# Performance work log

Measured on AMD Instinct MI355X. Metric: run time of the kernel, lower is better.

Reference implementation:

```python
import jax, jax.numpy as jnp
import numpy as np

B, C_IN, C_OUT, H, W = 4, 256, 256, 56, 56
NH, K, P = 2, 5, 2
HD = C_OUT // NH          # 128
SE_H = C_OUT // 16        # 16
SE_H2 = max(SE_H // 16, 1)  # 1
EPS = 1e-5


def setup_inputs() -> dict:
    key = jax.random.key(0)
    ks = jax.random.split(key, 16)
    n = lambda k, sh, s=1.0: jax.random.normal(k, sh, jnp.float32) * s

    def bn_params(k, c):
        k1, k2 = jax.random.split(k)
        return (1.0 + 0.1 * n(k1, (c,)), 0.1 * n(k2, (c,)),
                jnp.zeros((c,), jnp.float32), jnp.ones((c,), jnp.float32))

    agg_g1, agg_b1, agg_m1, agg_v1 = bn_params(ks[6], C_OUT)
    agg_g2, agg_b2, agg_m2, agg_v2 = bn_params(ks[7], C_OUT)
    se_g_in, se_b_in, se_m_in, se_v_in = bn_params(ks[8], SE_H)
    se_g_out, se_b_out, se_m_out, se_v_out = bn_params(ks[9], C_OUT)
    return {
        "x": n(ks[0], (B, C_IN, H, W)),
        "Wq": n(ks[1], (C_OUT, C_IN), C_IN ** -0.5),
        "Wk": n(ks[2], (C_OUT, C_IN), C_IN ** -0.5),
        "Wv": n(ks[3], (C_OUT, C_IN), C_IN ** -0.5),
        "rel_h": n(ks[4], (HD, 1, 1, K, 1)),
        "rel_w": n(ks[5], (HD, 1, 1, 1, K)),
        "agg_g1": agg_g1, "agg_b1": agg_b1, "agg_m1": agg_m1, "agg_v1": agg_v1,
        "agg_W": n(ks[10], (C_OUT, C_OUT), C_OUT ** -0.5),
        "agg_g2": agg_g2, "agg_b2": agg_b2, "agg_m2": agg_m2, "agg_v2": agg_v2,
        "se_Win": n(ks[11], (SE_H, C_OUT), C_OUT ** -0.5),
        "se_g_in": se_g_in, "se_b_in": se_b_in, "se_m_in": se_m_in, "se_v_in": se_v_in,
        "se_fc1": n(ks[12], (SE_H2, SE_H), SE_H ** -0.5),
        "se_fc2": n(ks[13], (SE_H, SE_H2)),
        "se_Wout": n(ks[14], (C_OUT, SE_H), SE_H ** -0.5),
        "se_g_out": se_g_out, "se_b_out": se_b_out, "se_m_out": se_m_out, "se_v_out": se_v_out,
    }


def _conv1x1(Wm, t):
    return jnp.einsum('oc,bchw->bohw', Wm, t)


def _bn(t, g, b, m, v):
    # eval-mode BatchNorm2d with running stats
    return (t - m[:, None, None]) * (g * jax.lax.rsqrt(v + EPS))[:, None, None] + b[:, None, None]


def _windows(t):
    # (B, O, H+2P, W+2P) -> (B, O, H, W, K, K), matching torch unfold(2,K,1).unfold(3,K,1)
    w = jnp.stack([t[:, :, i:i + H, j:j + W] for i in range(K) for j in range(K)], axis=-1)
    return w.reshape(t.shape[0], t.shape[1], H, W, K, K)


def reference(x, Wq, Wk, Wv, rel_h, rel_w,
              agg_g1, agg_b1, agg_m1, agg_v1, agg_W, agg_g2, agg_b2, agg_m2, agg_v2,
              se_Win, se_g_in, se_b_in, se_m_in, se_v_in, se_fc1, se_fc2, se_Wout,
              se_g_out, se_b_out, se_m_out, se_v_out):
    xp = jnp.pad(x, ((0, 0), (0, 0), (P, P), (P, P)))
    q = _conv1x1(Wq, x).reshape(B, NH, HD, H, W)          # (B,NH,HD,H,W)
    k_win = _windows(_conv1x1(Wk, xp))                    # (B,O,H,W,K,K)
    v_win = _windows(_conv1x1(Wv, xp))
    # relative position bias: first head gets rel_h (height taps), second gets rel_w
    k_win = jnp.concatenate([k_win[:, :HD] + rel_h[None], k_win[:, HD:] + rel_w[None]], axis=1)
    k_r = k_win.reshape(B, NH, HD, H, W, K * K)
    v_r = v_win.reshape(B, NH, HD, H, W, K * K)
    scores = jnp.einsum('bnchw,bnchwk->bnhwk', q, k_r) / jnp.sqrt(jnp.float32(HD))
    attn = jax.nn.softmax(scores, axis=-1)
    out = jnp.einsum('bnhwk,bnchwk->bnchw', attn, v_r).reshape(B, C_OUT, H, W)
    # agg: BN -> ReLU -> 1x1 conv -> BN
    y = jax.nn.relu(_bn(out, agg_g1, agg_b1, agg_m1, agg_v1))
    y = _bn(_conv1x1(agg_W, y), agg_g2, agg_b2, agg_m2, agg_v2)
    # squeeze-excitation (intended math; original view(b,c) is a channel-count bug)
    s = jax.nn.relu(_bn(_conv1x1(se_Win, y), se_g_in, se_b_in, se_m_in, se_v_in))  # (B,SE_H,H,W)
    p = s.mean(axis=(2, 3))                                                        # (B,SE_H)
    g = jax.nn.sigmoid(jax.nn.relu(p @ se_fc1.T) @ se_fc2.T)                       # (B,SE_H)
    s = s * g[:, :, None, None]
    return _bn(_conv1x1(se_Wout, s), se_g_out, se_b_out, se_m_out, se_v_out)
```

## Files before the change

kernel.cpp:

```cpp
#include <hip/hip_runtime.h>
#include <hip/hip_bf16.h>

#define HW 3136
#define HH 56
#define WW 56
#define BB 4
#define CC 256
#define HD 128

#define TH 4
#define TW 8
#define WR 8
#define WC 12
#define WPX 96
#define KSTR 132
#define SSTR 33

#define ASTR 72

typedef __attribute__((ext_vector_type(8))) short bf16x8;
typedef __attribute__((ext_vector_type(4))) float f32x4;

__device__ __forceinline__ unsigned short f2bf(float f) {
    unsigned int u; __builtin_memcpy(&u, &f, 4);
    unsigned int r = u + 0x7FFFu + ((u >> 16) & 1u);
    return (unsigned short)(r >> 16);
}
__device__ __forceinline__ float bflo(unsigned int u) {
    unsigned int x = u << 16; float f; __builtin_memcpy(&f, &x, 4); return f;
}
__device__ __forceinline__ float bfhi(unsigned int u) {
    unsigned int x = u & 0xFFFF0000u; float f; __builtin_memcpy(&f, &x, 4); return f;
}

__global__ __launch_bounds__(256) void xt_cvt(const float* __restrict__ x,
                                              unsigned short* __restrict__ xt)
{
    int b = blockIdx.z;
    int c0 = blockIdx.y * 64;
    int p0 = blockIdx.x * 64;
    __shared__ float tile[64][65];
    int t = threadIdx.x;
    int p4 = t & 15, cl = t >> 4;
    const float* xb = x + ((size_t)b * CC + c0) * HW + p0;
#pragma unroll
    for (int i = 0; i < 4; i++) {
        int c = cl + 16 * i;
        float4 f = *(const float4*)(xb + (size_t)c * HW + p4 * 4);
        tile[c][p4 * 4 + 0] = f.x; tile[c][p4 * 4 + 1] = f.y;
        tile[c][p4 * 4 + 2] = f.z; tile[c][p4 * 4 + 3] = f.w;
    }
    __syncthreads();
    int c2 = t & 31, pl = t >> 5;
    unsigned short* xo = xt + ((size_t)b * HW + p0) * CC + c0;
#pragma unroll
    for (int i = 0; i < 8; i++) {
        int p = pl + 8 * i;
        float a = tile[2 * c2][p], bb = tile[2 * c2 + 1][p];
        unsigned int pk = (unsigned int)f2bf(a) | ((unsigned int)f2bf(bb) << 16);
        *(unsigned int*)(xo + (size_t)p * CC + 2 * c2) = pk;
    }
}

__global__ __launch_bounds__(256) void wcvt(const float* __restrict__ Wq,
                                            const float* __restrict__ Wk,
                                            const float* __restrict__ Wv,
                                            const float* __restrict__ Wa,
                                            unsigned short* __restrict__ wb)
{
    const float* srcs[4] = {Wq, Wk, Wv, Wa};
    const float* s = srcs[blockIdx.y];
    int idx = blockIdx.x * 256 + threadIdx.x;
    float4 f = *(const float4*)(s + (size_t)idx * 4);
    uint2 pk;
    pk.x = (unsigned int)f2bf(f.x) | ((unsigned int)f2bf(f.y) << 16);
    pk.y = (unsigned int)f2bf(f.z) | ((unsigned int)f2bf(f.w) << 16);
    *(uint2*)(wb + (size_t)blockIdx.y * 65536 + (size_t)idx * 4) = pk;
}

__global__ __launch_bounds__(256) void qkv_mfma(
    const unsigned short* __restrict__ xt, const unsigned short* __restrict__ wqkv,
    unsigned short* __restrict__ q_ws, unsigned short* __restrict__ k_ws,
    unsigned short* __restrict__ v_ws)
{
    int wsel = blockIdx.z;
    unsigned short* outp = (wsel == 0) ? q_ws : ((wsel == 1) ? k_ws : v_ws);
    int gp0 = blockIdx.x * 128, o0 = blockIdx.y * 128;

    __shared__ unsigned short As[128 * ASTR];
    __shared__ unsigned short Bs[128 * ASTR];
    const unsigned short* xb = xt + (size_t)gp0 * CC;
    const unsigned short* wbp = wqkv + (size_t)wsel * 65536 + (size_t)o0 * CC;

    int t = threadIdx.x;
    int wave = t >> 6, lane = t & 63;
    int mo = (wave & 1) * 64, no = (wave >> 1) * 64;
    int lm = lane & 15, lq = lane >> 4;
    int sr = t >> 3, sc = t & 7;

    f32x4 acc[4][4];
#pragma unroll
    for (int i = 0; i < 4; i++)
#pragma unroll
        for (int j = 0; j < 4; j++) acc[i][j] = (f32x4){0.f, 0.f, 0.f, 0.f};

    for (int k0 = 0; k0 < 256; k0 += 64) {
#pragma unroll
        for (int i = 0; i < 4; i++) {
            int r = sr + 32 * i;
            *(uint4*)&As[r * ASTR + sc * 8] = *(const uint4*)(xb + (size_t)r * CC + k0 + sc * 8);
            *(uint4*)&Bs[r * ASTR + sc * 8] = *(const uint4*)(wbp + (size_t)r * CC + k0 + sc * 8);
        }
        __syncthreads();
#pragma unroll
        for (int ks = 0; ks < 64; ks += 32) {
            bf16x8 af[4], bfr[4];
#pragma unroll
            for (int i = 0; i < 4; i++)
                af[i] = *(bf16x8*)&As[(mo + 16 * i + lm) * ASTR + ks + lq * 8];
#pragma unroll
            for (int j = 0; j < 4; j++)
                bfr[j] = *(bf16x8*)&Bs[(no + 16 * j + lm) * ASTR + ks + lq * 8];
#pragma unroll
            for (int i = 0; i < 4; i++)
#pragma unroll
                for (int j = 0; j < 4; j++)
                    acc[i][j] = __builtin_amdgcn_mfma_f32_16x16x32_bf16(
                        af[i], bfr[j], acc[i][j], 0, 0, 0);
        }
        __syncthreads();
    }
    unsigned short* ob = outp + (size_t)gp0 * CC + o0;
    bool ev = (lm & 1) == 0;
    int elm = lm & ~1;
#pragma unroll
    for (int i = 0; i < 4; i++)
#pragma unroll
        for (int j = 0; j < 4; j++)
#pragma unroll
            for (int r = 0; r < 4; r++) {
                float v = acc[i][j][r];
                float p = __shfl_xor(v, 1, 64);
                unsigned int pk = ev
                    ? ((unsigned int)f2bf(v) | ((unsigned int)f2bf(p) << 16))
                    : ((unsigned int)f2bf(p) | ((unsigned int)f2bf(v) << 16));
                if (ev == (r < 2)) {
                    int m = mo + 16 * i + lq * 4 + r;
                    int n = no + 16 * j + elm;
                    *(unsigned int*)(ob + (size_t)m * CC + n) = pk;
                }
            }
}

__global__ __launch_bounds__(256) void agg_mfma(
    const unsigned short* __restrict__ ao, const unsigned short* __restrict__ wagg,
    const float* __restrict__ g1, const float* __restrict__ b1,
    const float* __restrict__ m1, const float* __restrict__ v1,
    const float* __restrict__ g2, const float* __restrict__ b2,
    const float* __restrict__ m2, const float* __restrict__ v2,
    float* __restrict__ y2)
{
    int gp0 = blockIdx.x * 128, o0 = blockIdx.y * 128;

    __shared__ unsigned short As[128 * ASTR];
    __shared__ unsigned short Bs[128 * ASTR];
    __shared__ float s1[256], o1[256], s2[256], o2[256];

    int t = threadIdx.x;
    {
        float sc1 = g1[t] * rsqrtf(v1[t] + 1e-5f);
        s1[t] = sc1; o1[t] = b1[t] - m1[t] * sc1;
        float sc2 = g2[t] * rsqrtf(v2[t] + 1e-5f);
        s2[t] = sc2; o2[t] = b2[t] - m2[t] * sc2;
    }

    const unsigned short* aob = ao + (size_t)gp0 * CC;
    const unsigned short* wbp = wagg + (size_t)o0 * CC;

    int wave = t >> 6, lane = t & 63;
    int mo = (wave & 1) * 64, no = (wave >> 1) * 64;
    int lm = lane & 15, lq = lane >> 4;
    int sr = t >> 3, sc = t & 7;

    f32x4 acc[4][4];
#pragma unroll
    for (int i = 0; i < 4; i++)
#pragma unroll
        for (int j = 0; j < 4; j++) acc[i][j] = (f32x4){0.f, 0.f, 0.f, 0.f};

    __syncthreads();

    for (int k0 = 0; k0 < 256; k0 += 64) {
#pragma unroll
        for (int i = 0; i < 4; i++) {
            int r = sr + 32 * i;
            int cb = k0 + sc * 8;
            uint4 u = *(const uint4*)(aob + (size_t)r * CC + cb);
            float e[8] = {bflo(u.x), bfhi(u.x), bflo(u.y), bfhi(u.y),
                          bflo(u.z), bfhi(u.z), bflo(u.w), bfhi(u.w)};
            unsigned short pk[8];
#pragma unroll
            for (int uu = 0; uu < 8; uu++) {
                float vv = fmaxf(e[uu] * s1[cb + uu] + o1[cb + uu], 0.f);
                pk[uu] = f2bf(vv);
            }
            *(uint4*)&As[r * ASTR + sc * 8] = *(uint4*)pk;
            *(uint4*)&Bs[r * ASTR + sc * 8] = *(const uint4*)(wbp + (size_t)r * CC + k0 + sc * 8);
        }
        __syncthreads();
#pragma unroll
        for (int ks = 0; ks < 64; ks += 32) {
            bf16x8 af[4], bfr[4];
#pragma unroll
            for (int i = 0; i < 4; i++)
                af[i] = *(bf16x8*)&As[(mo + 16 * i + lm) * ASTR + ks + lq * 8];
#pragma unroll
            for (int j = 0; j < 4; j++)
                bfr[j] = *(bf16x8*)&Bs[(no + 16 * j + lm) * ASTR + ks + lq * 8];
#pragma unroll
            for (int i = 0; i < 4; i++)
#pragma unroll
                for (int j = 0; j < 4; j++)
                    acc[i][j] = __builtin_amdgcn_mfma_f32_16x16x32_bf16(
                        af[i], bfr[j], acc[i][j], 0, 0, 0);
        }
        __syncthreads();
    }
    float* yb = y2 + (size_t)gp0 * CC + o0;
#pragma unroll
    for (int i = 0; i < 4; i++)
#pragma unroll
        for (int j = 0; j < 4; j++)
#pragma unroll
            for (int r = 0; r < 4; r++) {
                int m = mo + 16 * i + lq * 4 + r;
                int n = no + 16 * j + lm;
                yb[(size_t)m * CC + n] = acc[i][j][r] * s2[o0 + n] + o2[o0 + n];
            }
}

__global__ __launch_bounds__(256) void attn_kernel(
    const unsigned short* __restrict__ q_ws, const unsigned short* __restrict__ k_ws,
    const unsigned short* __restrict__ v_ws,
    const float* __restrict__ rel_h, const float* __restrict__ rel_w,
    unsigned short* __restrict__ ao_ws)
{
    __shared__ float kwin[WPX * KSTR];
    __shared__ float sbuf[32 * SSTR];
    __shared__ float relT[5 * KSTR];

    int t = threadIdx.x;
    int tile = blockIdx.x;
    int n = blockIdx.y;
    int b = blockIdx.z;
    int tr = tile / 7, tc = tile - tr * 7;
    int h0 = tr * TH, w0 = tc * TW;
    const float* rel = (n == 0) ? rel_h : rel_w;
    const size_t base = (size_t)b * HW * CC + n * HD;

    {
        int c8 = t & 15, pw0 = t >> 4;
#pragma unroll
        for (int it = 0; it < 6; it++) {
            int pw = pw0 + it * 16;
            int wr = pw / 12, wc = pw - wr * 12;
            int gh = h0 + wr - 2, gw = w0 + wc - 2;
            float f[8] = {0.f, 0.f, 0.f, 0.f, 0.f, 0.f, 0.f, 0.f};
            if (gh >= 0 && gh < HH && gw >= 0 && gw < WW) {
                uint4 u = *(const uint4*)(k_ws + base + (size_t)(gh * WW + gw) * CC + c8 * 8);
                f[0] = bflo(u.x); f[1] = bfhi(u.x); f[2] = bflo(u.y); f[3] = bfhi(u.y);
                f[4] = bflo(u.z); f[5] = bfhi(u.z); f[6] = bflo(u.w); f[7] = bfhi(u.w);
            }
            *(float4*)&kwin[pw * KSTR + c8 * 8]     = make_float4(f[0], f[1], f[2], f[3]);
            *(float4*)&kwin[pw * KSTR + c8 * 8 + 4] = make_float4(f[4], f[5], f[6], f[7]);
        }
        if (t < 128) {
#pragma unroll
            for (int tt = 0; tt < 5; tt++)
                relT[tt * KSTR + t] = rel[t * 5 + tt];
        }
    }
    __syncthreads();

    int px = t >> 3, c4g = t & 7;
    int pr = px >> 3, pc = px & 7;
    int ghp = h0 + pr, gwp = w0 + pc;
    const size_t pbase = base + (size_t)(ghp * WW + gwp) * CC;

    float4 q4[4];
#pragma unroll
    for (int i = 0; i < 4; i++) {
        uint2 uq = *(const uint2*)(q_ws + pbase + (c4g + 8 * i) * 4);
        q4[i] = make_float4(bflo(uq.x), bfhi(uq.x), bflo(uq.y), bfhi(uq.y));
    }

    float acc[30];
#pragma unroll
    for (int tt = 0; tt < 30; tt++) acc[tt] = 0.f;
#pragma unroll
    for (int i = 0; i < 4; i++) {
        float4 q = q4[i];
        int co = (c4g + 8 * i) * 4;
#pragma unroll
        for (int tt = 0; tt < 25; tt++) {
            int di = tt / 5, dj = tt - 5 * (tt / 5);
            int wpx = (pr + di) * WC + pc + dj;
            float4 k4 = *(const float4*)&kwin[wpx * KSTR + co];
            acc[tt] += q.x * k4.x + q.y * k4.y + q.z * k4.z + q.w * k4.w;
        }
#pragma unroll
        for (int tt = 0; tt < 5; tt++) {
            float4 r4 = *(const float4*)&relT[tt * KSTR + co];
            acc[25 + tt] += q.x * r4.x + q.y * r4.y + q.z * r4.z + q.w * r4.w;
        }
    }
#pragma unroll
    for (int tt = 0; tt < 30; tt++) {
#pragma unroll
        for (int m = 1; m < 8; m <<= 1)
            acc[tt] += __shfl_xor(acc[tt], m, 64);
    }
#pragma unroll
    for (int tt = 0; tt < 30; tt++)
        if ((tt & 7) == c4g) sbuf[px * SSTR + tt] = acc[tt];
    __syncthreads();

    {
        int c8 = t & 15, pw0 = t >> 4;
#pragma unroll
        for (int it = 0; it < 6; it++) {
            int pw = pw0 + it * 16;
            int wr = pw / 12, wc = pw - wr * 12;
            int gh = h0 + wr - 2, gw = w0 + wc - 2;
            float f[8] = {0.f, 0.f, 0.f, 0.f, 0.f, 0.f, 0.f, 0.f};
            if (gh >= 0 && gh < HH && gw >= 0 && gw < WW) {
                uint4 u = *(const uint4*)(v_ws + base + (size_t)(gh * WW + gw) * CC + c8 * 8);
                f[0] = bflo(u.x); f[1] = bfhi(u.x); f[2] = bflo(u.y); f[3] = bfhi(u.y);
                f[4] = bflo(u.z); f[5] = bfhi(u.z); f[6] = bflo(u.w); f[7] = bfhi(u.w);
            }
            *(float4*)&kwin[pw * KSTR + c8 * 8]     = make_float4(f[0], f[1], f[2], f[3]);
            *(float4*)&kwin[pw * KSTR + c8 * 8 + 4] = make_float4(f[4], f[5], f[6], f[7]);
        }
    }
    if (t < 32) {
        float s[25], b5[5];
#pragma unroll
        for (int tt = 0; tt < 25; tt++) s[tt] = sbuf[t * SSTR + tt];
#pragma unroll
        for (int tt = 0; tt < 5; tt++) b5[tt] = sbuf[t * SSTR + 25 + tt];
        const float inv = 0.08838834764831845f;
        float mx = -1e30f;
#pragma unroll
        for (int tt = 0; tt < 25; tt++) {
            int di = tt / 5, dj = tt - 5 * (tt / 5);
            s[tt] = (s[tt] + ((n == 0) ? b5[di] : b5[dj])) * inv;
            mx = fmaxf(mx, s[tt]);
        }
        float sum = 0.f;
#pragma unroll
        for (int tt = 0; tt < 25; tt++) { s[tt] = __expf(s[tt] - mx); sum += s[tt]; }
        float rs = 1.f / sum;
#pragma unroll
        for (int tt = 0; tt < 25; tt++) sbuf[t * SSTR + tt] = s[tt] * rs;
    }
    __syncthreads();

    float w25[25];
#pragma unroll
    for (int tt = 0; tt < 25; tt++) w25[tt] = sbuf[px * SSTR + tt];
    float4 oacc[4];
#pragma unroll
    for (int i = 0; i < 4; i++) oacc[i] = make_float4(0.f, 0.f, 0.f, 0.f);
#pragma unroll
    for (int tt = 0; tt < 25; tt++) {
        int di = tt / 5, dj = tt - 5 * (tt / 5);
        int wpx = (pr + di) * WC + pc + dj;
        float a = w25[tt];
#pragma unroll
        for (int i = 0; i < 4; i++) {
            float4 v4 = *(const float4*)&kwin[wpx * KSTR + (c4g + 8 * i) * 4];
            oacc[i].x += a * v4.x; oacc[i].y += a * v4.y;
            oacc[i].z += a * v4.z; oacc[i].w += a * v4.w;
        }
    }
#pragma unroll
    for (int i = 0; i < 4; i++) {
        uint2 pk;
        pk.x = (unsigned int)f2bf(oacc[i].x) | ((unsigned int)f2bf(oacc[i].y) << 16);
        pk.y = (unsigned int)f2bf(oacc[i].z) | ((unsigned int)f2bf(oacc[i].w) << 16);
        *(uint2*)(ao_ws + pbase + (c4g + 8 * i) * 4) = pk;
    }
}

__global__ __launch_bounds__(256) void se_in_kernel(
    const float* __restrict__ y2, const float* __restrict__ se_Win,
    const float* __restrict__ gin, const float* __restrict__ bin,
    const float* __restrict__ min_, const float* __restrict__ vin,
    float* __restrict__ s_ws, float* __restrict__ psum)
{
    int b = blockIdx.y;
    int p0 = blockIdx.x * 16;
    __shared__ float yt[16][257];
    __shared__ float wt[16][257];
    __shared__ float red[16][17];
    int t = threadIdx.x;
    const float* yb = y2 + (size_t)(b * HW + p0) * CC;
#pragma unroll
    for (int i = 0; i < 16; i++) yt[i][t] = yb[(size_t)i * CC + t];
#pragma unroll
    for (int i = 0; i < 16; i++) wt[i][t] = se_Win[i * 256 + t];
    __syncthreads();
    int p = t >> 4, j = t & 15;
    float dot = 0.f;
#pragma unroll 8
    for (int c = 0; c < 256; c++) dot += yt[p][c] * wt[j][c];
    float sc = gin[j] * rsqrtf(vin[j] + 1e-5f);
    float sv = fmaxf((dot - min_[j]) * sc + bin[j], 0.f);
    s_ws[(size_t)(b * HW + p0 + p) * 16 + j] = sv;
    red[p][j] = sv;
    __syncthreads();
    if (t < 16) {
        float sm = 0.f;
#pragma unroll
        for (int pp = 0; pp < 16; pp++) sm += red[pp][t];
        atomicAdd(&psum[b * 16 + t], sm);
    }
}

__global__ void zero64(float* p) { p[threadIdx.x] = 0.f; }

__global__ void se_gate(const float* __restrict__ psum,
                        const float* __restrict__ fc1,
                        const float* __restrict__ fc2,
                        float* __restrict__ g_ws)
{
    int t = threadIdx.x;
    if (t >= 64) return;
    int b = t >> 4, j = t & 15;
    float h = 0.f;
#pragma unroll
    for (int jj = 0; jj < 16; jj++)
        h += (psum[b * 16 + jj] * (1.f / 3136.f)) * fc1[jj];
    h = fmaxf(h, 0.f);
    float z = h * fc2[j];
    g_ws[t] = 1.f / (1.f + __expf(-z));
}

__global__ __launch_bounds__(256) void se_out_kernel(
    const float* __restrict__ s_ws, const float* __restrict__ g_ws,
    const float* __restrict__ se_Wout,
    const float* __restrict__ gout, const float* __restrict__ bout,
    const float* __restrict__ mout, const float* __restrict__ vout,
    float* __restrict__ out)
{
    int b = blockIdx.z;
    int o0 = blockIdx.y * 4;
    int p0 = blockIdx.x * 64;
    __shared__ float st[64][17];
    __shared__ float wg[4][16];
    int t = threadIdx.x;
#pragma unroll
    for (int i = 0; i < 4; i++) {
        int idx = i * 256 + t;
        st[idx >> 4][idx & 15] = s_ws[(size_t)(b * HW + p0 + (idx >> 4)) * 16 + (idx & 15)];
    }
    if (t < 64) {
        int ol = t >> 4, j = t & 15;
        wg[ol][j] = se_Wout[(o0 + ol) * 16 + j] * g_ws[b * 16 + j];
    }
    __syncthreads();
    int ol = t >> 6, pl = t & 63;
    float dot = 0.f;
#pragma unroll
    for (int j = 0; j < 16; j++) dot += st[pl][j] * wg[ol][j];
    int o = o0 + ol;
    float sc = gout[o] * rsqrtf(vout[o] + 1e-5f);
    float r = (dot - mout[o]) * sc + bout[o];
    out[((size_t)(b * 256 + o)) * HW + p0 + pl] = r;
}

extern "C" void kernel_launch(void* const* d_in, const int* in_sizes, int n_in,
                              void* d_out, int out_size, void* d_ws, size_t ws_size,
                              hipStream_t stream) {
    const float* x     = (const float*)d_in[0];
    const float* Wq    = (const float*)d_in[1];
    const float* Wk    = (const float*)d_in[2];
    const float* Wv    = (const float*)d_in[3];
    const float* rel_h = (const float*)d_in[4];
    const float* rel_w = (const float*)d_in[5];
    const float* agg_g1 = (const float*)d_in[6];
    const float* agg_b1 = (const float*)d_in[7];
    const float* agg_m1 = (const float*)d_in[8];
    const float* agg_v1 = (const float*)d_in[9];
    const float* agg_W  = (const float*)d_in[10];
    const float* agg_g2 = (const float*)d_in[11];
    const float* agg_b2 = (const float*)d_in[12];
    const float* agg_m2 = (const float*)d_in[13];
    const float* agg_v2 = (const float*)d_in[14];
    const float* se_Win = (const float*)d_in[15];
    const float* se_g_in = (const float*)d_in[16];
    const float* se_b_in = (const float*)d_in[17];
    const float* se_m_in = (const float*)d_in[18];
    const float* se_v_in = (const float*)d_in[19];
    const float* se_fc1  = (const float*)d_in[20];
    const float* se_fc2  = (const float*)d_in[21];
    const float* se_Wout = (const float*)d_in[22];
    const float* se_g_out = (const float*)d_in[23];
    const float* se_b_out = (const float*)d_in[24];
    const float* se_m_out = (const float*)d_in[25];
    const float* se_v_out = (const float*)d_in[26];

    const size_t NQ = (size_t)BB * HW * CC;
    unsigned short* q_ws  = (unsigned short*)d_ws;
    unsigned short* k_ws  = q_ws + NQ;
    unsigned short* v_ws  = k_ws + NQ;
    unsigned short* ao_ws = v_ws + NQ;
    unsigned short* xt    = ao_ws;
    float* y2_ws = (float*)d_ws;
    float* s_ws  = (float*)(ao_ws + NQ);
    float* psum  = s_ws + (size_t)BB * HW * 16;
    float* g_ws  = psum + 64;
    unsigned short* wbf = (unsigned short*)(g_ws + 64);

    xt_cvt<<<dim3(49, 4, 4), 256, 0, stream>>>(x, xt);
    wcvt<<<dim3(64, 4), 256, 0, stream>>>(Wq, Wk, Wv, agg_W, wbf);
    qkv_mfma<<<dim3(98, 2, 3), 256, 0, stream>>>(xt, wbf, q_ws, k_ws, v_ws);
    attn_kernel<<<dim3(98, 2, 4), 256, 0, stream>>>(q_ws, k_ws, v_ws, rel_h, rel_w, ao_ws);
    agg_mfma<<<dim3(98, 2), 256, 0, stream>>>(ao_ws, wbf + 3 * 65536,
        agg_g1, agg_b1, agg_m1, agg_v1, agg_g2, agg_b2, agg_m2, agg_v2, y2_ws);
    zero64<<<1, 64, 0, stream>>>(psum);
    se_in_kernel<<<dim3(196, 4), 256, 0, stream>>>(y2_ws, se_Win,
        se_g_in, se_b_in, se_m_in, se_v_in, s_ws, psum);
    se_gate<<<1, 64, 0, stream>>>(psum, se_fc1, se_fc2, g_ws);
    se_out_kernel<<<dim3(49, 64, 4), 256, 0, stream>>>(s_ws, g_ws, se_Wout,
        se_g_out, se_b_out, se_m_out, se_v_out, (float*)d_out);
}
```

Measured before the change: 206.6 us.

## Fuse softmax into attention registers, use MFMA for SE-in, merge SE gate and zeroing

Attention now computes the softmax redundantly in every lane's registers after the shuffle reduction, dropping the shared score buffer and one barrier. The SE input projection becomes a bf16 MFMA kernel, with the weight converted in the existing weight-convert kernel, which now also zeroes the pooled sums. The gate computation moves into the SE output kernel, which is restructured so each block handles 32 pixels across all 256 output channels. Two tiny launches disappear, in exchange for bf16 rounding in the SE projection and each SE-out block recomputing the gate.

```diff
diff --git a/kernel.cpp b/kernel.cpp
--- a/kernel.cpp
+++ b/kernel.cpp
@@ -14,7 +14,6 @@
 #define WC 12
 #define WPX 96
 #define KSTR 132
-#define SSTR 33
 
 #define ASTR 72
 
@@ -66,11 +65,26 @@
                                             const float* __restrict__ Wk,
                                             const float* __restrict__ Wv,
                                             const float* __restrict__ Wa,
-                                            unsigned short* __restrict__ wb)
-{
+                                            const float* __restrict__ Wse,
+                                            unsigned short* __restrict__ wb,
+                                            float* __restrict__ psum)
+{
+    int t = threadIdx.x;
+    if (blockIdx.y == 4) {
+        if (blockIdx.x == 0 && t < 64) psum[t] = 0.f;
+        int idx = blockIdx.x * 256 + t;
+        if (idx < 1024) {
+            float4 f = *(const float4*)(Wse + (size_t)idx * 4);
+            uint2 pk;
+            pk.x = (unsigned int)f2bf(f.x) | ((unsigned int)f2bf(f.y) << 16);
+            pk.y = (unsigned int)f2bf(f.z) | ((unsigned int)f2bf(f.w) << 16);
+            *(uint2*)(wb + (size_t)4 * 65536 + (size_t)idx * 4) = pk;
+        }
+        return;
+    }
     const float* srcs[4] = {Wq, Wk, Wv, Wa};
     const float* s = srcs[blockIdx.y];
-    int idx = blockIdx.x * 256 + threadIdx.x;
+    int idx = blockIdx.x * 256 + t;
     float4 f = *(const float4*)(s + (size_t)idx * 4);
     uint2 pk;
     pk.x = (unsigned int)f2bf(f.x) | ((unsigned int)f2bf(f.y) << 16);
@@ -246,7 +260,6 @@
     unsigned short* __restrict__ ao_ws)
 {
     __shared__ float kwin[WPX * KSTR];
-    __shared__ float sbuf[32 * SSTR];
     __shared__ float relT[5 * KSTR];
 
     int t = threadIdx.x;
@@ -320,9 +333,22 @@
         for (int m = 1; m < 8; m <<= 1)
             acc[tt] += __shfl_xor(acc[tt], m, 64);
     }
-#pragma unroll
-    for (int tt = 0; tt < 30; tt++)
-        if ((tt & 7) == c4g) sbuf[px * SSTR + tt] = acc[tt];
+    {
+        const float inv = 0.08838834764831845f;
+        float mx = -1e30f;
+#pragma unroll
+        for (int tt = 0; tt < 25; tt++) {
+            int di = tt / 5, dj = tt - 5 * (tt / 5);
+            acc[tt] = (acc[tt] + ((n == 0) ? acc[25 + di] : acc[25 + dj])) * inv;
+            mx = fmaxf(mx, acc[tt]);
+        }
+        float sum = 0.f;
+#pragma unroll
+        for (int tt = 0; tt < 25; tt++) { acc[tt] = __expf(acc[tt] - mx); sum += acc[tt]; }
+        float rs = 1.f / sum;
+#pragma unroll
+        for (int tt = 0; tt < 25; tt++) acc[tt] *= rs;
+    }
     __syncthreads();
 
     {
@@ -342,32 +368,8 @@
             *(float4*)&kwin[pw * KSTR + c8 * 8 + 4] = make_float4(f[4], f[5], f[6], f[7]);
         }
     }
-    if (t < 32) {
-        float s[25], b5[5];
-#pragma unroll
-        for (int tt = 0; tt < 25; tt++) s[tt] = sbuf[t * SSTR + tt];
-#pragma unroll
-        for (int tt = 0; tt < 5; tt++) b5[tt] = sbuf[t * SSTR + 25 + tt];
-        const float inv = 0.08838834764831845f;
-        float mx = -1e30f;
-#pragma unroll
-        for (int tt = 0; tt < 25; tt++) {
-            int di = tt / 5, dj = tt - 5 * (tt / 5);
-            s[tt] = (s[tt] + ((n == 0) ? b5[di] : b5[dj])) * inv;
-            mx = fmaxf(mx, s[tt]);
-        }
-        float sum = 0.f;
-#pragma unroll
-        for (int tt = 0; tt < 25; tt++) { s[tt] = __expf(s[tt] - mx); sum += s[tt]; }
-        float rs = 1.f / sum;
-#pragma unroll
-        for (int tt = 0; tt < 25; tt++) sbuf[t * SSTR + tt] = s[tt] * rs;
-    }
-    __syncthreads();
-
-    float w25[25];
-#pragma unroll
-    for (int tt = 0; tt < 25; tt++) w25[tt] = sbuf[px * SSTR + tt];
+    __syncthreads();
+
     float4 oacc[4];
 #pragma unroll
     for (int i = 0; i < 4; i++) oacc[i] = make_float4(0.f, 0.f, 0.f, 0.f);
@@ -375,7 +377,7 @@
     for (int tt = 0; tt < 25; tt++) {
         int di = tt / 5, dj = tt - 5 * (tt / 5);
         int wpx = (pr + di) * WC + pc + dj;
-        float a = w25[tt];
+        float a = acc[tt];
 #pragma unroll
         for (int i = 0; i < 4; i++) {
             float4 v4 = *(const float4*)&kwin[wpx * KSTR + (c4g + 8 * i) * 4];
@@ -392,91 +394,110 @@
     }
 }
 
-__global__ __launch_bounds__(256) void se_in_kernel(
-    const float* __restrict__ y2, const float* __restrict__ se_Win,
+__global__ __launch_bounds__(256) void se_in_mfma(
+    const float* __restrict__ y2, const unsigned short* __restrict__ wse,
     const float* __restrict__ gin, const float* __restrict__ bin,
     const float* __restrict__ min_, const float* __restrict__ vin,
     float* __restrict__ s_ws, float* __restrict__ psum)
 {
-    int b = blockIdx.y;
-    int p0 = blockIdx.x * 16;
-    __shared__ float yt[16][257];
-    __shared__ float wt[16][257];
-    __shared__ float red[16][17];
-    int t = threadIdx.x;
-    const float* yb = y2 + (size_t)(b * HW + p0) * CC;
-#pragma unroll
-    for (int i = 0; i < 16; i++) yt[i][t] = yb[(size_t)i * CC + t];
-#pragma unroll
-    for (int i = 0; i < 16; i++) wt[i][t] = se_Win[i * 256 + t];
-    __syncthreads();
-    int p = t >> 4, j = t & 15;
-    float dot = 0.f;
-#pragma unroll 8
-    for (int c = 0; c < 256; c++) dot += yt[p][c] * wt[j][c];
-    float sc = gin[j] * rsqrtf(vin[j] + 1e-5f);
-    float sv = fmaxf((dot - min_[j]) * sc + bin[j], 0.f);
-    s_ws[(size_t)(b * HW + p0 + p) * 16 + j] = sv;
-    red[p][j] = sv;
-    __syncthreads();
-    if (t < 16) {
-        float sm = 0.f;
-#pragma unroll
-        for (int pp = 0; pp < 16; pp++) sm += red[pp][t];
-        atomicAdd(&psum[b * 16 + t], sm);
-    }
-}
-
-__global__ void zero64(float* p) { p[threadIdx.x] = 0.f; }
-
-__global__ void se_gate(const float* __restrict__ psum,
-                        const float* __restrict__ fc1,
-                        const float* __restrict__ fc2,
-                        float* __restrict__ g_ws)
-{
-    int t = threadIdx.x;
-    if (t >= 64) return;
-    int b = t >> 4, j = t & 15;
-    float h = 0.f;
-#pragma unroll
-    for (int jj = 0; jj < 16; jj++)
-        h += (psum[b * 16 + jj] * (1.f / 3136.f)) * fc1[jj];
-    h = fmaxf(h, 0.f);
-    float z = h * fc2[j];
-    g_ws[t] = 1.f / (1.f + __expf(-z));
+    int wave = threadIdx.x >> 6, lane = threadIdx.x & 63;
+    int tile = blockIdx.x * 4 + wave;
+    int gp0 = tile * 16;
+    int b = tile / 196;
+    int lm = lane & 15, lq = lane >> 4;
+
+    f32x4 acc = (f32x4){0.f, 0.f, 0.f, 0.f};
+    const float* ya = y2 + (size_t)(gp0 + lm) * CC;
+#pragma unroll
+    for (int k0 = 0; k0 < 256; k0 += 32) {
+        int kb = k0 + lq * 8;
+        float4 f0 = *(const float4*)(ya + kb);
+        float4 f1 = *(const float4*)(ya + kb + 4);
+        unsigned short pk[8] = {f2bf(f0.x), f2bf(f0.y), f2bf(f0.z), f2bf(f0.w),
+                                f2bf(f1.x), f2bf(f1.y), f2bf(f1.z), f2bf(f1.w)};
+        bf16x8 af = *(bf16x8*)pk;
+        bf16x8 bf = *(const bf16x8*)(wse + (size_t)lm * CC + kb);
+        acc = __builtin_amdgcn_mfma_f32_16x16x32_bf16(af, bf, acc, 0, 0, 0);
+    }
+    float sc = gin[lm] * rsqrtf(vin[lm] + 1e-5f);
+    float off = bin[lm] - min_[lm] * sc;
+    float sum4 = 0.f;
+#pragma unroll
+    for (int r = 0; r < 4; r++) {
+        int row = lq * 4 + r;
+        float v = fmaxf(acc[r] * sc + off, 0.f);
+        s_ws[(size_t)(gp0 + row) * 16 + lm] = v;
+        sum4 += v;
+    }
+    sum4 += __shfl_xor(sum4, 16, 64);
+    sum4 += __shfl_xor(sum4, 32, 64);
+    if (lane < 16) atomicAdd(&psum[b * 16 + lane], sum4);
 }
 
 __global__ __launch_bounds__(256) void se_out_kernel(
-    const float* __restrict__ s_ws, const float* __restrict__ g_ws,
+    const float* __restrict__ s_ws, const float* __restrict__ psum,
+    const float* __restrict__ fc1, const float* __restrict__ fc2,
     const float* __restrict__ se_Wout,
     const float* __restrict__ gout, const float* __restrict__ bout,
     const float* __restrict__ mout, const float* __restrict__ vout,
     float* __restrict__ out)
 {
-    int b = blockIdx.z;
-    int o0 = blockIdx.y * 4;
-    int p0 = blockIdx.x * 64;
-    __shared__ float st[64][17];
-    __shared__ float wg[4][16];
+    int b = blockIdx.y;
+    int px0 = blockIdx.x * 32;
+    __shared__ float sl[32 * 17];
+    __shared__ float wg[256 * 20];
+    __shared__ float bo[256];
+    __shared__ float gg[16];
     int t = threadIdx.x;
-#pragma unroll
-    for (int i = 0; i < 4; i++) {
-        int idx = i * 256 + t;
-        st[idx >> 4][idx & 15] = s_ws[(size_t)(b * HW + p0 + (idx >> 4)) * 16 + (idx & 15)];
-    }
-    if (t < 64) {
-        int ol = t >> 4, j = t & 15;
-        wg[ol][j] = se_Wout[(o0 + ol) * 16 + j] * g_ws[b * 16 + j];
-    }
-    __syncthreads();
-    int ol = t >> 6, pl = t & 63;
-    float dot = 0.f;
-#pragma unroll
-    for (int j = 0; j < 16; j++) dot += st[pl][j] * wg[ol][j];
-    int o = o0 + ol;
-    float sc = gout[o] * rsqrtf(vout[o] + 1e-5f);
-    float r = (dot - mout[o]) * sc + bout[o];
-    out[((size_t)(b * 256 + o)) * HW + p0 + pl] = r;
+
+    if (t < 16) {
+        float h = 0.f;
+#pragma unroll
+        for (int jj = 0; jj < 16; jj++)
+            h += (psum[b * 16 + jj] * (1.f / 3136.f)) * fc1[jj];
+        h = fmaxf(h, 0.f);
+        float z = h * fc2[t];
+        gg[t] = 1.f / (1.f + __expf(-z));
+    }
+    {
+        const float* sb = s_ws + (size_t)(b * HW + px0) * 16;
+#pragma unroll
+        for (int i = 0; i < 2; i++) {
+            int idx = t + 256 * i;
+            sl[(idx >> 4) * 17 + (idx & 15)] = sb[idx];
+        }
+    }
+    __syncthreads();
+    {
+        float sc = gout[t] * rsqrtf(vout[t] + 1e-5f);
+        bo[t] = bout[t] - mout[t] * sc;
+        const float* wr = se_Wout + (size_t)t * 16;
+#pragma unroll
+        for (int k = 0; k < 16; k++)
+            wg[t * 20 + k] = wr[k] * gg[k] * sc;
+    }
+    __syncthreads();
+
+    int px = t & 31, og = t >> 5;
+    float4 s0 = *(float4*)&sl[px * 17 + 0];
+    float4 s1v = *(float4*)&sl[px * 17 + 4];
+    float4 s2v = *(float4*)&sl[px * 17 + 8];
+    float4 s3 = *(float4*)&sl[px * 17 + 12];
+    float* ob = out + (size_t)b * CC * HW + px0 + px;
+#pragma unroll
+    for (int oi = 0; oi < 32; oi++) {
+        int o = og * 32 + oi;
+        float4 w0 = *(float4*)&wg[o * 20 + 0];
+        float4 w1 = *(float4*)&wg[o * 20 + 4];
+        float4 w2 = *(float4*)&wg[o * 20 + 8];
+        float4 w3 = *(float4*)&wg[o * 20 + 12];
+        float r = bo[o]
+            + s0.x * w0.x + s0.y * w0.y + s0.z * w0.z + s0.w * w0.w
+            + s1v.x * w1.x + s1v.y * w1.y + s1v.z * w1.z + s1v.w * w1.w
+            + s2v.x * w2.x + s2v.y * w2.y + s2v.z * w2.z + s2v.w * w2.w
+            + s3.x * w3.x + s3.y * w3.y + s3.z * w3.z + s3.w * w3.w;
+        ob[(size_t)o * HW] = r;
+    }
 }
 
 extern "C" void kernel_launch(void* const* d_in, const int* in_sizes, int n_in,
@@ -519,19 +540,16 @@
     float* y2_ws = (float*)d_ws;
     float* s_ws  = (float*)(ao_ws + NQ);
     float* psum  = s_ws + (size_t)BB * HW * 16;
-    float* g_ws  = psum + 64;
-    unsigned short* wbf = (unsigned short*)(g_ws + 64);
+    unsigned short* wbf = (unsigned short*)(psum + 64);
 
     xt_cvt<<<dim3(49, 4, 4), 256, 0, stream>>>(x, xt);
-    wcvt<<<dim3(64, 4), 256, 0, stream>>>(Wq, Wk, Wv, agg_W, wbf);
+    wcvt<<<dim3(64, 5), 256, 0, stream>>>(Wq, Wk, Wv, agg_W, se_Win, wbf, psum);
     qkv_mfma<<<dim3(98, 2, 3), 256, 0, stream>>>(xt, wbf, q_ws, k_ws, v_ws);
     attn_kernel<<<dim3(98, 2, 4), 256, 0, stream>>>(q_ws, k_ws, v_ws, rel_h, rel_w, ao_ws);
     agg_mfma<<<dim3(98, 2), 256, 0, stream>>>(ao_ws, wbf + 3 * 65536,
         agg_g1, agg_b1, agg_m1, agg_v1, agg_g2, agg_b2, agg_m2, agg_v2, y2_ws);
-    zero64<<<1, 64, 0, stream>>>(psum);
-    se_in_kernel<<<dim3(196, 4), 256, 0, stream>>>(y2_ws, se_Win,
+    se_in_mfma<<<dim3(196), 256, 0, stream>>>(y2_ws, wbf + 4 * 65536,
         se_g_in, se_b_in, se_m_in, se_v_in, s_ws, psum);
-    se_gate<<<1, 64, 0, stream>>>(psum, se_fc1, se_fc2, g_ws);
-    se_out_kernel<<<dim3(49, 64, 4), 256, 0, stream>>>(s_ws, g_ws, se_Wout,
-        se_g_out, se_b_out, se_m_out, se_v_out, (float*)d_out);
-}
+    se_out_kernel<<<dim3(98, 4), 256, 0, stream>>>(s_ws, psum, se_fc1, se_fc2,
+        se_Wout, se_g_out, se_b_out, se_m_out, se_v_out, (float*)d_out);
+}
```

After: 197.0 us. 4.7% less time.
